# Kernel optimization log

Measured on AMD Instinct MI355X. Metric: run time of the kernel, lower is better.

Reference implementation:

```python
import jax, jax.numpy as jnp
import numpy as np

NUM_HEADS = 8
WEIGHTS_DIM = 512
INPUT_DIM = 512
D_HEAD = WEIGHTS_DIM // NUM_HEADS


def setup_inputs() -> dict:
    key = jax.random.key(0)
    ks = jax.random.split(key, 9)
    B, S, D = 4, 2048, INPUT_DIM
    s_in = 1.0 / np.sqrt(D)
    s_w = 1.0 / np.sqrt(WEIGHTS_DIM)
    return {
        "x": jax.random.normal(ks[0], (B, S, D), dtype=jnp.float32),
        "Wq": jax.random.normal(ks[1], (D, WEIGHTS_DIM), dtype=jnp.float32) * s_in,
        "bq": jnp.zeros((WEIGHTS_DIM,), dtype=jnp.float32),
        "Wk": jax.random.normal(ks[2], (D, WEIGHTS_DIM), dtype=jnp.float32) * s_in,
        "bk": jnp.zeros((WEIGHTS_DIM,), dtype=jnp.float32),
        "Wv": jax.random.normal(ks[3], (D, WEIGHTS_DIM), dtype=jnp.float32) * s_in,
        "bv": jnp.zeros((WEIGHTS_DIM,), dtype=jnp.float32),
        "Wh": jax.random.normal(ks[4], (WEIGHTS_DIM, D), dtype=jnp.float32) * s_w,
        "bh": jnp.zeros((D,), dtype=jnp.float32),
    }


def _split_heads(t):
    # [B, S, Dm] -> [B, H, S, d_head]
    B, S, _ = t.shape
    return t.reshape(B, S, NUM_HEADS, D_HEAD).transpose(0, 2, 1, 3)


def reference(x, Wq, bq, Wk, bk, Wv, bv, Wh, bh):
    q = _split_heads(x @ Wq + bq)
    k = _split_heads(x @ Wk + bk)
    v = _split_heads(x @ Wv + bv)
    scale = 1.0 / jnp.sqrt(jnp.float32(D_HEAD))
    scores = jnp.einsum("bhqd,bhkd->bhqk", q, k) * scale  # [B,H,S,S]
    weights = jax.nn.softmax(scores, axis=-1)
    attn = jnp.einsum("bhqk,bhkd->bhqd", weights, v)
    B, H, S, d = attn.shape
    concat = attn.transpose(0, 2, 1, 3).reshape(B, S, H * d)
    return concat @ Wh + bh
```

## Files before the change

kernel.cpp:

```cpp
#include <hip/hip_runtime.h>
#include <stdint.h>

#define NB  4
#define SS  2048
#define DD  512
#define HH  8
#define DHH 64
#define MM  (NB * SS)

typedef __attribute__((ext_vector_type(8))) short bf16x8;
typedef __attribute__((ext_vector_type(4))) float f32x4;
typedef __attribute__((ext_vector_type(4))) short s16x4;

union fu32 { float f; unsigned u; };
union pfu  { uint4 u; bf16x8 v; };

static __device__ __forceinline__ short f2bf(float f) {
  fu32 a; a.f = f;
  unsigned u = a.u;
  return (short)((u + 0x7fffu + ((u >> 16) & 1u)) >> 16);
}
static __device__ __forceinline__ float bf2f(short s) {
  fu32 t; t.u = ((unsigned)(unsigned short)s) << 16;
  return t.f;
}

static __device__ __forceinline__ void async16(const void* g, void* l) {
  __builtin_amdgcn_global_load_lds(
      (__attribute__((address_space(1))) unsigned*)(void*)g,
      (__attribute__((address_space(3))) unsigned*)l, 16, 0, 0);
}

__global__ __launch_bounds__(256) void prep_kernel(
    const float* __restrict__ x, short* __restrict__ xb,
    const float* __restrict__ W0, const float* __restrict__ W1,
    const float* __restrict__ W2, const float* __restrict__ W3,
    short* __restrict__ T0, short* __restrict__ T1,
    short* __restrict__ T2, short* __restrict__ T3) {
  const int bid = blockIdx.x, tid = threadIdx.x;
  if (bid < 2048) {
    int i = (bid * 256 + tid) * 8;
    float4 v0 = *(const float4*)(x + i);
    float4 v1 = *(const float4*)(x + i + 4);
    bf16x8 o;
    o[0] = f2bf(v0.x); o[1] = f2bf(v0.y); o[2] = f2bf(v0.z); o[3] = f2bf(v0.w);
    o[4] = f2bf(v1.x); o[5] = f2bf(v1.y); o[6] = f2bf(v1.z); o[7] = f2bf(v1.w);
    *(bf16x8*)(xb + i) = o;
  } else {
    int z = bid - 2048;
    int widx = z >> 6, rem = z & 63;
    const float* W = widx == 0 ? W0 : widx == 1 ? W1 : widx == 2 ? W2 : W3;
    short*       T = widx == 0 ? T0 : widx == 1 ? T1 : widx == 2 ? T2 : T3;
    int n  = (rem & 7) * 64 + (tid & 63);
    int k0 = (rem >> 3) * 64 + (tid >> 6) * 16;
    bf16x8 t0, t1;
#pragma unroll
    for (int j = 0; j < 8; ++j) t0[j] = f2bf(W[(size_t)(k0 + j) * DD + n]);
#pragma unroll
    for (int j = 0; j < 8; ++j) t1[j] = f2bf(W[(size_t)(k0 + 8 + j) * DD + n]);
    *(bf16x8*)(T + (size_t)n * DD + k0)     = t0;
    *(bf16x8*)(T + (size_t)n * DD + k0 + 8) = t1;
  }
}

__global__ __launch_bounds__(256, 4) void gemm_qkv_kernel(
    const short* __restrict__ A, const short* __restrict__ Bt,
    const float* __restrict__ bq, const float* __restrict__ bk,
    const float* __restrict__ bv, short* __restrict__ qout,
    short* __restrict__ kout, short* __restrict__ vtout, float qscale) {
  __shared__ __align__(16) short sh[64 * 64 + 128 * 64];
  short* a_sh = sh;
  short* b_sh = sh + 64 * 64;
  const int tid  = threadIdx.x;
  const int w    = tid >> 6, lane = tid & 63, quad = lane >> 4, l16 = lane & 15;
  const int m0   = blockIdx.y * 64, n0 = blockIdx.x * 128;
  const int mw   = (w >> 1) * 32,   nw = (w & 1) * 64;
  const int rw   = lane >> 3, seg = lane & 7, gs = seg ^ rw;
  const int sxz  = l16 & 7;

  f32x4 acc[2][4];
#pragma unroll
  for (int i = 0; i < 2; ++i)
#pragma unroll
    for (int j = 0; j < 4; ++j) acc[i][j] = {0.f, 0.f, 0.f, 0.f};

  for (int kt = 0; kt < DD; kt += 64) {
    __syncthreads();
    {
      const short* ga = A  + (size_t)(m0 + w * 16 + rw) * DD + kt + gs * 8;
      const short* gb = Bt + (size_t)(n0 + w * 32 + rw) * DD + kt + gs * 8;
#pragma unroll
      for (int i = 0; i < 2; ++i)
        async16(ga + (size_t)i * 8 * DD, &a_sh[(w * 16 + i * 8) * 64]);
#pragma unroll
      for (int i = 0; i < 4; ++i)
        async16(gb + (size_t)i * 8 * DD, &b_sh[(w * 32 + i * 8) * 64]);
    }
    __syncthreads();
#pragma unroll
    for (int ks = 0; ks < 2; ++ks) {
      const int so = ((ks * 4 + quad) ^ sxz) * 8;
      bf16x8 af[2], bfr[4];
#pragma unroll
      for (int mt = 0; mt < 2; ++mt)
        af[mt] = *(const bf16x8*)&a_sh[(mw + mt * 16 + l16) * 64 + so];
#pragma unroll
      for (int nt = 0; nt < 4; ++nt)
        bfr[nt] = *(const bf16x8*)&b_sh[(nw + nt * 16 + l16) * 64 + so];
#pragma unroll
      for (int mt = 0; mt < 2; ++mt)
#pragma unroll
        for (int nt = 0; nt < 4; ++nt)
          acc[mt][nt] = __builtin_amdgcn_mfma_f32_16x16x32_bf16(
              af[mt], bfr[nt], acc[mt][nt], 0, 0, 0);
    }
  }

  __syncthreads();
  const int sgb = n0 >> 9;
  const int h0  = (n0 & 511) >> 6;
  const int bi  = m0 >> 11, s0 = m0 & (SS - 1);
  if (sgb < 2) {
    const float* bias = (sgb == 0) ? bq : bk;
    const float  scl  = (sgb == 0) ? qscale : 1.0f;
#pragma unroll
    for (int nt = 0; nt < 4; ++nt) {
      const int dl = nw + nt * 16 + l16;
      const float bval = bias[(n0 & 511) + dl];
#pragma unroll
      for (int mt = 0; mt < 2; ++mt)
#pragma unroll
        for (int r = 0; r < 4; ++r)
          sh[(mw + mt * 16 + quad * 4 + r) * 136 + dl] =
              f2bf((acc[mt][nt][r] + bval) * scl);
    }
    __syncthreads();
    short* o = (sgb == 0) ? qout : kout;
#pragma unroll
    for (int i = 0; i < 4; ++i) {
      const int c = tid + 256 * i;
      const int s = c >> 4, d8 = (c & 15) * 8;
      const int hh = h0 + (d8 >> 6), dd = d8 & 63;
      *(bf16x8*)&o[((size_t)(bi * HH + hh) * SS + s0 + s) * DHH + dd] =
          *(const bf16x8*)&sh[s * 136 + d8];
    }
  } else {
#pragma unroll
    for (int nt = 0; nt < 4; ++nt) {
      const int dl = nw + nt * 16 + l16;
      const float bval = bv[(n0 & 511) + dl];
#pragma unroll
      for (int mt = 0; mt < 2; ++mt)
#pragma unroll
        for (int r = 0; r < 4; ++r)
          sh[dl * 72 + mw + mt * 16 + quad * 4 + r] = f2bf(acc[mt][nt][r] + bval);
    }
    __syncthreads();
#pragma unroll
    for (int i = 0; i < 4; ++i) {
      const int c = tid + 256 * i;
      const int d = c >> 3, s8 = (c & 7) * 8;
      const int hh = h0 + (d >> 6), dd = d & 63;
      *(bf16x8*)&vtout[((size_t)(bi * HH + hh) * DHH + dd) * SS + s0 + s8] =
          *(const bf16x8*)&sh[d * 72 + s8];
    }
  }
}

__global__ __launch_bounds__(256, 2) void attn_kernel(
    const short* __restrict__ Qa, const short* __restrict__ Ka,
    const short* __restrict__ Vt, short* __restrict__ Op0,
    short* __restrict__ Op1, float* __restrict__ lpw) {
  __shared__ __align__(16) short k_sh[256 * 64];
  __shared__ __align__(16) short vt_sh[64 * 256];

  const int tid  = threadIdx.x;
  const int w    = tid >> 6, lane = tid & 63, quad = lane >> 4, l16 = lane & 15;
  const int n    = blockIdx.x;
  const int grp  = (n & 7) * 8 + ((n >> 3) & 7);
  const int qt_b = n >> 6;
  const int half = grp & 1, h = (grp >> 1) & 7, b = grp >> 4;
  const int q0   = qt_b * 256;
  const int rw = lane >> 3, seg = lane & 7, gs = seg ^ rw;
  const int sxz = l16 & 7;
  const size_t base = (size_t)(b * HH + h) * SS * DHH;
  const short* Qg = Qa + base + (size_t)(q0 + w * 64) * DHH;
  const short* Kg = Ka + base;
  const short* Vg = Vt + base;

  bf16x8 qf[4][2];
#pragma unroll
  for (int qt = 0; qt < 4; ++qt)
#pragma unroll
    for (int ks = 0; ks < 2; ++ks)
      qf[qt][ks] = *(const bf16x8*)(Qg + (size_t)(qt * 16 + l16) * DHH + ks * 32 + quad * 8);

  bf16x8 ones;
#pragma unroll
  for (int j = 0; j < 8; ++j) ones[j] = (short)0x3F80;

  f32x4 o_acc[4][4];
#pragma unroll
  for (int qt = 0; qt < 4; ++qt)
#pragma unroll
    for (int dt = 0; dt < 4; ++dt) o_acc[qt][dt] = {0.f, 0.f, 0.f, 0.f};
  f32x4 l_acc[4];
#pragma unroll
  for (int qt = 0; qt < 4; ++qt) l_acc[qt] = {0.f, 0.f, 0.f, 0.f};

  const int addrA = ((((quad & 1) << 1) + (quad >> 1)) * 16 + l16) * 4;
  const int addrB = addrA ^ 64;
  const bool qeven = (quad & 1) == 0;

  const int kstart = half * (SS / 2);

  for (int kb = kstart; kb < kstart + SS / 2; kb += 256) {
    __syncthreads();
    {
      const short* gk = Kg + (size_t)(kb + w * 64 + rw) * DHH + gs * 8;
#pragma unroll
      for (int i = 0; i < 8; ++i)
        async16(gk + (size_t)i * 8 * DHH, &k_sh[(w * 64 + i * 8) * 64]);
#pragma unroll
      for (int i = 0; i < 8; ++i) {
        const int d = w * 16 + i * 2 + (lane >> 5);
        const int kseg = (lane & 31) ^ (d & 31);
        async16(Vg + (size_t)d * SS + kb + kseg * 8,
                &vt_sh[(w * 16 + i * 2) * 256]);
      }
    }
    __syncthreads();

#pragma unroll
    for (int ck = 0; ck < 8; ++ck) {
      uint2 pk[4][2];
#pragma unroll
      for (int t = 0; t < 2; ++t) {
        const int knt = ck * 2 + t;
        bf16x8 kf0 = *(const bf16x8*)&k_sh[(knt * 16 + l16) * 64 + ((0 * 4 + quad) ^ sxz) * 8];
        bf16x8 kf1 = *(const bf16x8*)&k_sh[(knt * 16 + l16) * 64 + ((1 * 4 + quad) ^ sxz) * 8];
#pragma unroll
        for (int qt = 0; qt < 4; ++qt) {
          f32x4 s = {0.f, 0.f, 0.f, 0.f};
          s = __builtin_amdgcn_mfma_f32_16x16x32_bf16(kf0, qf[qt][0], s, 0, 0, 0);
          s = __builtin_amdgcn_mfma_f32_16x16x32_bf16(kf1, qf[qt][1], s, 0, 0, 0);
          fu32 e0, e1, e2, e3;
          e0.f = __builtin_amdgcn_exp2f(s[0]);
          e1.f = __builtin_amdgcn_exp2f(s[1]);
          e2.f = __builtin_amdgcn_exp2f(s[2]);
          e3.f = __builtin_amdgcn_exp2f(s[3]);
          pk[qt][t].x = __builtin_amdgcn_perm(e1.u, e0.u, 0x07060302u);
          pk[qt][t].y = __builtin_amdgcn_perm(e3.u, e2.u, 0x07060302u);
        }
      }
      bf16x8 vf[4];
#pragma unroll
      for (int dt = 0; dt < 4; ++dt) {
        const int dl = dt * 16 + l16;
        vf[dt] = *(const bf16x8*)&vt_sh[dl * 256 + ((ck * 4 + quad) ^ (dl & 31)) * 8];
      }
#pragma unroll
      for (int qt = 0; qt < 4; ++qt) {
        unsigned p1x = (unsigned)__shfl_xor((int)pk[qt][1].x, 16);
        unsigned p1y = (unsigned)__shfl_xor((int)pk[qt][1].y, 16);
        unsigned v0x = qeven ? pk[qt][0].x : p1x;
        unsigned v0y = qeven ? pk[qt][0].y : p1y;
        unsigned v2x = qeven ? p1x : pk[qt][0].x;
        unsigned v2y = qeven ? p1y : pk[qt][0].y;
        pfu pf;
        pf.u.x = (unsigned)__builtin_amdgcn_ds_bpermute(addrA, (int)v0x);
        pf.u.y = (unsigned)__builtin_amdgcn_ds_bpermute(addrA, (int)v0y);
        pf.u.z = (unsigned)__builtin_amdgcn_ds_bpermute(addrB, (int)v2x);
        pf.u.w = (unsigned)__builtin_amdgcn_ds_bpermute(addrB, (int)v2y);
        l_acc[qt] = __builtin_amdgcn_mfma_f32_16x16x32_bf16(pf.v, ones, l_acc[qt], 0, 0, 0);
#pragma unroll
        for (int dt = 0; dt < 4; ++dt)
          o_acc[qt][dt] = __builtin_amdgcn_mfma_f32_16x16x32_bf16(pf.v, vf[dt], o_acc[qt][dt], 0, 0, 0);
      }
    }
  }

  short* Op = half ? Op1 : Op0;
#pragma unroll
  for (int qt = 0; qt < 4; ++qt) {
#pragma unroll
    for (int r = 0; r < 4; ++r) {
      const int qg = q0 + w * 64 + qt * 16 + quad * 4 + r;
      const size_t row = (size_t)(b * HH + h) * SS + qg;
      if (l16 == 0)
        lpw[(size_t)half * (NB * HH * SS) + row] = l_acc[qt][r];
      const float inv = __builtin_amdgcn_rcpf(l_acc[qt][r]);
#pragma unroll
      for (int dt = 0; dt < 4; ++dt)
        Op[row * DHH + dt * 16 + l16] = f2bf(o_acc[qt][dt][r] * inv);
    }
  }
}

__global__ __launch_bounds__(256, 4) void gemm_proj_kernel(
    const short* __restrict__ Op0, const short* __restrict__ Op1,
    const float* __restrict__ lpw, const short* __restrict__ Bt,
    const float* __restrict__ bias, float* __restrict__ out) {
  __shared__ __align__(16) short a0_sh[64 * 64];
  __shared__ __align__(16) short a1_sh[64 * 64];
  __shared__ __align__(16) short b_sh[64 * 64];
  const int tid = threadIdx.x;
  const int w   = tid >> 6, lane = tid & 63, quad = lane >> 4, l16 = lane & 15;
  const int m0  = blockIdx.y * 64, n0 = blockIdx.x * 64;
  const int mw  = (w >> 1) * 32, nw = (w & 1) * 32;
  const int rw  = lane >> 3, seg = lane & 7, gs = seg ^ rw;
  const int sxz = l16 & 7;
  const int bb  = m0 >> 11, q0 = m0 & (SS - 1);

  f32x4 acc[2][2];
#pragma unroll
  for (int i = 0; i < 2; ++i)
#pragma unroll
    for (int j = 0; j < 2; ++j) acc[i][j] = {0.f, 0.f, 0.f, 0.f};

  for (int kt = 0; kt < DD; kt += 64) {
    const int h = kt >> 6;
    const size_t lbase = (size_t)(bb * HH + h) * SS + q0;
    const size_t abase = lbase * DHH;
    __syncthreads();
    {
      const short* g0 = Op0 + abase + (size_t)(w * 16 + rw) * DHH + gs * 8;
      const short* g1 = Op1 + abase + (size_t)(w * 16 + rw) * DHH + gs * 8;
      const short* gb = Bt + (size_t)(n0 + w * 16 + rw) * DD + kt + gs * 8;
#pragma unroll
      for (int i = 0; i < 2; ++i) {
        async16(g0 + (size_t)i * 8 * DHH, &a0_sh[(w * 16 + i * 8) * 64]);
        async16(g1 + (size_t)i * 8 * DHH, &a1_sh[(w * 16 + i * 8) * 64]);
        async16(gb + (size_t)i * 8 * DD,  &b_sh[(w * 16 + i * 8) * 64]);
      }
    }
    float w1[2], w2[2];
#pragma unroll
    for (int mt = 0; mt < 2; ++mt) {
      const size_t lrow = lbase + mw + mt * 16 + l16;
      const float l1 = lpw[lrow];
      const float l2 = lpw[(size_t)NB * HH * SS + lrow];
      const float inv = __builtin_amdgcn_rcpf(l1 + l2);
      w1[mt] = l1 * inv; w2[mt] = l2 * inv;
    }
    __syncthreads();
#pragma unroll
    for (int ks = 0; ks < 2; ++ks) {
      const int so = ((ks * 4 + quad) ^ sxz) * 8;
      pfu af[2];
#pragma unroll
      for (int mt = 0; mt < 2; ++mt) {
        bf16x8 a0 = *(const bf16x8*)&a0_sh[(mw + mt * 16 + l16) * 64 + so];
        bf16x8 a1 = *(const bf16x8*)&a1_sh[(mw + mt * 16 + l16) * 64 + so];
        unsigned* rp = (unsigned*)&af[mt];
#pragma unroll
        for (int jp = 0; jp < 4; ++jp) {
          fu32 f0, f1;
          f0.f = w1[mt] * bf2f(a0[2 * jp])     + w2[mt] * bf2f(a1[2 * jp]);
          f1.f = w1[mt] * bf2f(a0[2 * jp + 1]) + w2[mt] * bf2f(a1[2 * jp + 1]);
          rp[jp] = __builtin_amdgcn_perm(f1.u, f0.u, 0x07060302u);
        }
      }
#pragma unroll
      for (int nt = 0; nt < 2; ++nt) {
        bf16x8 bfr = *(const bf16x8*)&b_sh[(nw + nt * 16 + l16) * 64 + so];
        acc[0][nt] = __builtin_amdgcn_mfma_f32_16x16x32_bf16(af[0].v, bfr, acc[0][nt], 0, 0, 0);
        acc[1][nt] = __builtin_amdgcn_mfma_f32_16x16x32_bf16(af[1].v, bfr, acc[1][nt], 0, 0, 0);
      }
    }
  }

#pragma unroll
  for (int nt = 0; nt < 2; ++nt) {
    const int   n  = n0 + nw + nt * 16 + l16;
    const float bv = bias[n];
#pragma unroll
    for (int mt = 0; mt < 2; ++mt)
#pragma unroll
      for (int r = 0; r < 4; ++r) {
        const int m = m0 + mw + mt * 16 + quad * 4 + r;
        out[(size_t)m * DD + n] = acc[mt][nt][r] + bv;
      }
  }
}

extern "C" void kernel_launch(void* const* d_in, const int* in_sizes, int n_in,
                              void* d_out, int out_size, void* d_ws, size_t ws_size,
                              hipStream_t stream) {
  (void)in_sizes; (void)n_in; (void)out_size; (void)ws_size;
  const float* x  = (const float*)d_in[0];
  const float* Wq = (const float*)d_in[1];
  const float* bq = (const float*)d_in[2];
  const float* Wk = (const float*)d_in[3];
  const float* bk = (const float*)d_in[4];
  const float* Wv = (const float*)d_in[5];
  const float* bv = (const float*)d_in[6];
  const float* Wh = (const float*)d_in[7];
  const float* bh = (const float*)d_in[8];

  short* ws  = (short*)d_ws;
  short* xb  = ws;
  short* wqt = xb  + (size_t)MM * DD;
  short* wkt = wqt + (size_t)DD * DD;
  short* wvt = wkt + (size_t)DD * DD;
  short* wht = wvt + (size_t)DD * DD;
  short* qws = wht + (size_t)DD * DD;
  short* kws = qws + (size_t)MM * DD;
  short* vws = kws + (size_t)MM * DD;
  short* op1 = vws + (size_t)MM * DD;
  float* lpw = (float*)(op1 + (size_t)MM * DD);

  hipLaunchKernelGGL(prep_kernel, dim3(2048 + 256), dim3(256), 0, stream,
                     x, xb, Wq, Wk, Wv, Wh, wqt, wkt, wvt, wht);

  const float qscale = 1.4426950408889634f / 8.0f;
  hipLaunchKernelGGL(gemm_qkv_kernel, dim3(12, 128), dim3(256), 0, stream,
                     xb, wqt, bq, bk, bv, qws, kws, vws, qscale);

  hipLaunchKernelGGL(attn_kernel, dim3(512), dim3(256), 0, stream,
                     qws, kws, vws, xb, op1, lpw);

  hipLaunchKernelGGL(gemm_proj_kernel, dim3(8, 128), dim3(256), 0, stream,
                     xb, op1, lpw, wht, bh, (float*)d_out);
}
```

Baseline: 171.8 us.

## Split attention keys into four partitions and combine partials in projection GEMM

The attention kernel now splits the key sequence into four quarters instead of two, doubling the grid to 1024 blocks, and halves the K/V shared-memory tiles to 128 keys so four blocks can be resident per CU. The projection GEMM loads four partial outputs and their row sums and combines them with normalized weights before the MFMA. This aims to raise occupancy and latency hiding in attention, but it adds workspace traffic and extra combine work in the projection kernel.

```diff
diff --git a/kernel.cpp b/kernel.cpp
--- a/kernel.cpp
+++ b/kernel.cpp
@@ -7,6 +7,7 @@
 #define HH  8
 #define DHH 64
 #define MM  (NB * SS)
+#define NHS (NB * HH * SS)
 
 typedef __attribute__((ext_vector_type(8))) short bf16x8;
 typedef __attribute__((ext_vector_type(4))) float f32x4;
@@ -167,19 +168,20 @@
   }
 }
 
-__global__ __launch_bounds__(256, 2) void attn_kernel(
+__global__ __launch_bounds__(256, 4) void attn_kernel(
     const short* __restrict__ Qa, const short* __restrict__ Ka,
     const short* __restrict__ Vt, short* __restrict__ Op0,
-    short* __restrict__ Op1, float* __restrict__ lpw) {
-  __shared__ __align__(16) short k_sh[256 * 64];
-  __shared__ __align__(16) short vt_sh[64 * 256];
+    short* __restrict__ Op1, short* __restrict__ Op2,
+    short* __restrict__ Op3, float* __restrict__ lpw) {
+  __shared__ __align__(16) short k_sh[128 * 64];
+  __shared__ __align__(16) short vt_sh[64 * 128];
 
   const int tid  = threadIdx.x;
   const int w    = tid >> 6, lane = tid & 63, quad = lane >> 4, l16 = lane & 15;
   const int n    = blockIdx.x;
-  const int grp  = (n & 7) * 8 + ((n >> 3) & 7);
-  const int qt_b = n >> 6;
-  const int half = grp & 1, h = (grp >> 1) & 7, b = grp >> 4;
+  const int grp  = (n & 7) * 16 + ((n >> 3) & 15);
+  const int qt_b = n >> 7;
+  const int quarter = grp & 3, h = (grp >> 2) & 7, b = grp >> 5;
   const int q0   = qt_b * 256;
   const int rw = lane >> 3, seg = lane & 7, gs = seg ^ rw;
   const int sxz = l16 & 7;
@@ -212,27 +214,27 @@
   const int addrB = addrA ^ 64;
   const bool qeven = (quad & 1) == 0;
 
-  const int kstart = half * (SS / 2);
-
-  for (int kb = kstart; kb < kstart + SS / 2; kb += 256) {
+  const int kstart = quarter * (SS / 4);
+
+  for (int kb = kstart; kb < kstart + SS / 4; kb += 128) {
     __syncthreads();
     {
-      const short* gk = Kg + (size_t)(kb + w * 64 + rw) * DHH + gs * 8;
-#pragma unroll
-      for (int i = 0; i < 8; ++i)
-        async16(gk + (size_t)i * 8 * DHH, &k_sh[(w * 64 + i * 8) * 64]);
-#pragma unroll
-      for (int i = 0; i < 8; ++i) {
-        const int d = w * 16 + i * 2 + (lane >> 5);
-        const int kseg = (lane & 31) ^ (d & 31);
-        async16(Vg + (size_t)d * SS + kb + kseg * 8,
-                &vt_sh[(w * 16 + i * 2) * 256]);
-      }
-    }
-    __syncthreads();
-
-#pragma unroll
-    for (int ck = 0; ck < 8; ++ck) {
+      const short* gk = Kg + (size_t)(kb + w * 32 + rw) * DHH + gs * 8;
+#pragma unroll
+      for (int i = 0; i < 4; ++i)
+        async16(gk + (size_t)i * 8 * DHH, &k_sh[(w * 32 + i * 8) * 64]);
+#pragma unroll
+      for (int i = 0; i < 4; ++i) {
+        const int d = w * 16 + i * 4 + (lane >> 4);
+        const int gseg = (lane & 15) ^ (d & 15);
+        async16(Vg + (size_t)d * SS + kb + gseg * 8,
+                &vt_sh[(w * 16 + i * 4) * 128]);
+      }
+    }
+    __syncthreads();
+
+#pragma unroll
+    for (int ck = 0; ck < 4; ++ck) {
       uint2 pk[4][2];
 #pragma unroll
       for (int t = 0; t < 2; ++t) {
@@ -257,7 +259,7 @@
 #pragma unroll
       for (int dt = 0; dt < 4; ++dt) {
         const int dl = dt * 16 + l16;
-        vf[dt] = *(const bf16x8*)&vt_sh[dl * 256 + ((ck * 4 + quad) ^ (dl & 31)) * 8];
+        vf[dt] = *(const bf16x8*)&vt_sh[dl * 128 + ((ck * 4 + quad) ^ (dl & 15)) * 8];
       }
 #pragma unroll
       for (int qt = 0; qt < 4; ++qt) {
@@ -280,7 +282,8 @@
     }
   }
 
-  short* Op = half ? Op1 : Op0;
+  short* Op = (quarter == 0) ? Op0 : (quarter == 1) ? Op1
+            : (quarter == 2) ? Op2 : Op3;
 #pragma unroll
   for (int qt = 0; qt < 4; ++qt) {
 #pragma unroll
@@ -288,7 +291,7 @@
       const int qg = q0 + w * 64 + qt * 16 + quad * 4 + r;
       const size_t row = (size_t)(b * HH + h) * SS + qg;
       if (l16 == 0)
-        lpw[(size_t)half * (NB * HH * SS) + row] = l_acc[qt][r];
+        lpw[(size_t)quarter * NHS + row] = l_acc[qt][r];
       const float inv = __builtin_amdgcn_rcpf(l_acc[qt][r]);
 #pragma unroll
       for (int dt = 0; dt < 4; ++dt)
@@ -299,10 +302,10 @@
 
 __global__ __launch_bounds__(256, 4) void gemm_proj_kernel(
     const short* __restrict__ Op0, const short* __restrict__ Op1,
+    const short* __restrict__ Op2, const short* __restrict__ Op3,
     const float* __restrict__ lpw, const short* __restrict__ Bt,
     const float* __restrict__ bias, float* __restrict__ out) {
-  __shared__ __align__(16) short a0_sh[64 * 64];
-  __shared__ __align__(16) short a1_sh[64 * 64];
+  __shared__ __align__(16) short a_sh[4][64 * 64];
   __shared__ __align__(16) short b_sh[64 * 64];
   const int tid = threadIdx.x;
   const int w   = tid >> 6, lane = tid & 63, quad = lane >> 4, l16 = lane & 15;
@@ -324,24 +327,28 @@
     const size_t abase = lbase * DHH;
     __syncthreads();
     {
-      const short* g0 = Op0 + abase + (size_t)(w * 16 + rw) * DHH + gs * 8;
-      const short* g1 = Op1 + abase + (size_t)(w * 16 + rw) * DHH + gs * 8;
+      const size_t off = abase + (size_t)(w * 16 + rw) * DHH + gs * 8;
       const short* gb = Bt + (size_t)(n0 + w * 16 + rw) * DD + kt + gs * 8;
 #pragma unroll
       for (int i = 0; i < 2; ++i) {
-        async16(g0 + (size_t)i * 8 * DHH, &a0_sh[(w * 16 + i * 8) * 64]);
-        async16(g1 + (size_t)i * 8 * DHH, &a1_sh[(w * 16 + i * 8) * 64]);
-        async16(gb + (size_t)i * 8 * DD,  &b_sh[(w * 16 + i * 8) * 64]);
-      }
-    }
-    float w1[2], w2[2];
+        async16(Op0 + off + (size_t)i * 8 * DHH, &a_sh[0][(w * 16 + i * 8) * 64]);
+        async16(Op1 + off + (size_t)i * 8 * DHH, &a_sh[1][(w * 16 + i * 8) * 64]);
+        async16(Op2 + off + (size_t)i * 8 * DHH, &a_sh[2][(w * 16 + i * 8) * 64]);
+        async16(Op3 + off + (size_t)i * 8 * DHH, &a_sh[3][(w * 16 + i * 8) * 64]);
+        async16(gb + (size_t)i * 8 * DD, &b_sh[(w * 16 + i * 8) * 64]);
+      }
+    }
+    float wq[4][2];
 #pragma unroll
     for (int mt = 0; mt < 2; ++mt) {
       const size_t lrow = lbase + mw + mt * 16 + l16;
-      const float l1 = lpw[lrow];
-      const float l2 = lpw[(size_t)NB * HH * SS + lrow];
-      const float inv = __builtin_amdgcn_rcpf(l1 + l2);
-      w1[mt] = l1 * inv; w2[mt] = l2 * inv;
+      const float l0 = lpw[lrow];
+      const float l1 = lpw[(size_t)NHS + lrow];
+      const float l2 = lpw[2 * (size_t)NHS + lrow];
+      const float l3 = lpw[3 * (size_t)NHS + lrow];
+      const float inv = __builtin_amdgcn_rcpf((l0 + l1) + (l2 + l3));
+      wq[0][mt] = l0 * inv; wq[1][mt] = l1 * inv;
+      wq[2][mt] = l2 * inv; wq[3][mt] = l3 * inv;
     }
     __syncthreads();
 #pragma unroll
@@ -350,14 +357,19 @@
       pfu af[2];
 #pragma unroll
       for (int mt = 0; mt < 2; ++mt) {
-        bf16x8 a0 = *(const bf16x8*)&a0_sh[(mw + mt * 16 + l16) * 64 + so];
-        bf16x8 a1 = *(const bf16x8*)&a1_sh[(mw + mt * 16 + l16) * 64 + so];
+        const int ro = (mw + mt * 16 + l16) * 64 + so;
+        bf16x8 a0 = *(const bf16x8*)&a_sh[0][ro];
+        bf16x8 a1 = *(const bf16x8*)&a_sh[1][ro];
+        bf16x8 a2 = *(const bf16x8*)&a_sh[2][ro];
+        bf16x8 a3 = *(const bf16x8*)&a_sh[3][ro];
         unsigned* rp = (unsigned*)&af[mt];
 #pragma unroll
         for (int jp = 0; jp < 4; ++jp) {
           fu32 f0, f1;
-          f0.f = w1[mt] * bf2f(a0[2 * jp])     + w2[mt] * bf2f(a1[2 * jp]);
-          f1.f = w1[mt] * bf2f(a0[2 * jp + 1]) + w2[mt] * bf2f(a1[2 * jp + 1]);
+          f0.f = wq[0][mt] * bf2f(a0[2 * jp])     + wq[1][mt] * bf2f(a1[2 * jp])
+               + wq[2][mt] * bf2f(a2[2 * jp])     + wq[3][mt] * bf2f(a3[2 * jp]);
+          f1.f = wq[0][mt] * bf2f(a0[2 * jp + 1]) + wq[1][mt] * bf2f(a1[2 * jp + 1])
+               + wq[2][mt] * bf2f(a2[2 * jp + 1]) + wq[3][mt] * bf2f(a3[2 * jp + 1]);
           rp[jp] = __builtin_amdgcn_perm(f1.u, f0.u, 0x07060302u);
         }
       }
@@ -408,7 +420,9 @@
   short* kws = qws + (size_t)MM * DD;
   short* vws = kws + (size_t)MM * DD;
   short* op1 = vws + (size_t)MM * DD;
-  float* lpw = (float*)(op1 + (size_t)MM * DD);
+  short* op2 = op1 + (size_t)MM * DD;
+  short* op3 = op2 + (size_t)MM * DD;
+  float* lpw = (float*)(op3 + (size_t)MM * DD);
 
   hipLaunchKernelGGL(prep_kernel, dim3(2048 + 256), dim3(256), 0, stream,
                      x, xb, Wq, Wk, Wv, Wh, wqt, wkt, wvt, wht);
@@ -417,9 +431,9 @@
   hipLaunchKernelGGL(gemm_qkv_kernel, dim3(12, 128), dim3(256), 0, stream,
                      xb, wqt, bq, bk, bv, qws, kws, vws, qscale);
 
-  hipLaunchKernelGGL(attn_kernel, dim3(512), dim3(256), 0, stream,
-                     qws, kws, vws, xb, op1, lpw);
+  hipLaunchKernelGGL(attn_kernel, dim3(1024), dim3(256), 0, stream,
+                     qws, kws, vws, xb, op1, op2, op3, lpw);
 
   hipLaunchKernelGGL(gemm_proj_kernel, dim3(8, 128), dim3(256), 0, stream,
-                     xb, op1, lpw, wht, bh, (float*)d_out);
-}
+                     xb, op1, op2, op3, lpw, wht, bh, (float*)d_out);
+}
```

New measurement: 548.4 us. +219.1%, slower.
